# Kernel optimization log

Hardware: AMD Instinct MI355X
Metric: run time of the kernel (lower is better)

## Reference

```python
import jax, jax.numpy as jnp
import numpy as np

ALPHA = 0.2  # LeakyReLU negative slope


def setup_inputs() -> dict:
    key = jax.random.key(0)
    k1, k2, k3, k4 = jax.random.split(key, 4)
    N, Fin, Fout = 8192, 256, 64
    inputs = {
        "input": jax.random.normal(k1, (N, Fin), dtype=jnp.float32),
        "adj": jax.random.randint(k2, (N, N), 0, 2, dtype=jnp.int32),
        "W": jax.random.normal(k3, (Fin, Fout), dtype=jnp.float32) * (1.414 * np.sqrt(2.0 / (Fin + Fout))),
        "a": jax.random.normal(k4, (2 * Fout, 1), dtype=jnp.float32) * (1.414 * np.sqrt(2.0 / (2 * Fout + 1))),
    }
    return inputs


def reference(input, adj, W, a):
    # h: [N, Fout]
    h = input @ W
    Fout = h.shape[1]
    # Decompose pairwise score: e[i,j] = leakyrelu(h[i]@a1 + h[j]@a2)
    # (mathematically identical to the original concat+matmul construction,
    #  but avoids the O(N^2 * 2F) intermediate)
    a1, a2 = a[:Fout, 0], a[Fout:, 0]
    s1 = h @ a1  # [N]
    s2 = h @ a2  # [N]
    e = jax.nn.leaky_relu(s1[:, None] + s2[None, :], negative_slope=ALPHA)  # [N, N]
    # Mask non-edges with -10 (as in the original), row softmax
    masked = jnp.where(adj > 0, e, jnp.float32(-10.0))
    attention = jax.nn.softmax(masked, axis=1)
    # dropout p=0.0 (eval/reference mode): identity
    h_prime = attention @ h  # [N, Fout]
    return jax.nn.elu(h_prime)  # concat=True path
```

## Files before the change

kernel.cpp:

```cpp
#include <hip/hip_runtime.h>
#include <hip/hip_bf16.h>
#include <cstdint>
#include <cstddef>

#define NN 8192
#define FIN 256
#define FOUT 64
#define ALPHA_SLOPE 0.2f
#define EXP_M10 4.5399929762484854e-05f

#define JSPLIT 2
#define JT 1024
#define NTILE ((NN / JSPLIT) / JT)
#define CP 68

typedef short s16x8 __attribute__((ext_vector_type(8)));
typedef float f32x4 __attribute__((ext_vector_type(4)));
typedef int   i32x4 __attribute__((ext_vector_type(4)));

__device__ __forceinline__ unsigned short f2bf(float x) {
    union { float f; uint32_t u; } v; v.f = x;
    uint32_t u = v.u;
    return (unsigned short)((u + 0x7FFFu + ((u >> 16) & 1u)) >> 16);
}

__device__ __forceinline__ int wt_off(int row, int chunk) {
    return row * JT + (((chunk) ^ (row & 7)) << 3);
}

__global__ __launch_bounds__(256) void k_h(
    const float* __restrict__ input, const float* __restrict__ W,
    const float* __restrict__ a,
    unsigned short* __restrict__ htg, float* __restrict__ s1, float* __restrict__ s2)
{
    __shared__ __align__(16) unsigned short tile[64][28];
    const int wid  = threadIdx.x >> 6;
    const int lane = threadIdx.x & 63;
    const int i0   = blockIdx.x * 16;
    const int r0   = wid * 4;
    const float* inb = input + (size_t)(i0 + r0) * FIN;

    float acc0 = 0.f, acc1 = 0.f, acc2 = 0.f, acc3 = 0.f;
    #pragma unroll 4
    for (int c = 0; c < FIN; c += 4) {
        float w0 = W[(c + 0) * FOUT + lane];
        float w1 = W[(c + 1) * FOUT + lane];
        float w2 = W[(c + 2) * FOUT + lane];
        float w3 = W[(c + 3) * FOUT + lane];
        float4 x0 = *(const float4*)(inb + 0 * FIN + c);
        float4 x1 = *(const float4*)(inb + 1 * FIN + c);
        float4 x2 = *(const float4*)(inb + 2 * FIN + c);
        float4 x3 = *(const float4*)(inb + 3 * FIN + c);
        acc0 = fmaf(x0.x, w0, fmaf(x0.y, w1, fmaf(x0.z, w2, fmaf(x0.w, w3, acc0))));
        acc1 = fmaf(x1.x, w0, fmaf(x1.y, w1, fmaf(x1.z, w2, fmaf(x1.w, w3, acc1))));
        acc2 = fmaf(x2.x, w0, fmaf(x2.y, w1, fmaf(x2.z, w2, fmaf(x2.w, w3, acc2))));
        acc3 = fmaf(x3.x, w0, fmaf(x3.y, w1, fmaf(x3.z, w2, fmaf(x3.w, w3, acc3))));
    }

    const float a1v = a[lane], a2v = a[FOUT + lane];
    float accs[4] = {acc0, acc1, acc2, acc3};
    #pragma unroll
    for (int r = 0; r < 4; ++r) {
        float v1 = accs[r] * a1v;
        float v2 = accs[r] * a2v;
        #pragma unroll
        for (int off = 32; off; off >>= 1) {
            v1 += __shfl_xor(v1, off);
            v2 += __shfl_xor(v2, off);
        }
        if (lane == 0) { s1[i0 + r0 + r] = v1; s2[i0 + r0 + r] = v2; }
        tile[lane][r0 + r] = f2bf(accs[r]);
    }
    __syncthreads();

    const int feat = threadIdx.x >> 2;
    const int cg   = (threadIdx.x & 3) * 4;
    uint2 q = *(const uint2*)&tile[feat][cg];
    *(uint2*)(htg + (size_t)feat * NN + i0 + cg) = q;
}

__global__ __launch_bounds__(256, 4) void k_attn(
    const int* __restrict__ adj,
    const unsigned short* __restrict__ htg,
    const float* __restrict__ s1g, const float* __restrict__ s2g,
    float* __restrict__ slabs)
{
    __shared__ __align__(16) unsigned short Wt[16 * JT];

    const int t    = threadIdx.x;
    const int wid  = t >> 6;
    const int lane = t & 63;
    const int bi   = blockIdx.x >> 1;
    const int js   = blockIdx.x & 1;
    const int i0   = bi * 16;
    const int jbase = js * (NN / JSPLIT);
    const int m    = lane & 15;
    const int quad = lane >> 4;

    const int srow = wid * 4;
    float s1r[4];
    #pragma unroll
    for (int r = 0; r < 4; ++r) s1r[r] = s1g[i0 + srow + r];

    const int kq = wid * (JT / 4);

    const short bd = (m == 0) ? (short)0x3F80 : (short)0;
    const s16x8 bden = {bd, bd, bd, bd, bd, bd, bd, bd};

    f32x4 acc0 = {0,0,0,0}, acc1 = {0,0,0,0}, acc2 = {0,0,0,0},
          acc3 = {0,0,0,0}, acc4 = {0,0,0,0};

    for (int tile = 0; tile < NTILE; ++tile) {
        const int j0 = jbase + tile * JT;
        __syncthreads();

        #pragma unroll
        for (int rr = 0; rr < 4; ++rr) {
            const int row = srow + rr;
            const int* ap = adj + (size_t)(i0 + row) * NN + j0;
            const float s1v = s1r[rr];
            #pragma unroll
            for (int c = 0; c < 4; ++c) {
                const int cc = c * 256 + lane * 4;
                i32x4  av = *(const i32x4*)(ap + cc);
                float4 sv = *(const float4*)(s2g + j0 + cc);
                float x0 = s1v + sv.x, x1 = s1v + sv.y;
                float x2 = s1v + sv.z, x3 = s1v + sv.w;
                float w0 = (av.x > 0) ? __expf(fmaxf(x0, ALPHA_SLOPE * x0)) : EXP_M10;
                float w1 = (av.y > 0) ? __expf(fmaxf(x1, ALPHA_SLOPE * x1)) : EXP_M10;
                float w2 = (av.z > 0) ? __expf(fmaxf(x2, ALPHA_SLOPE * x2)) : EXP_M10;
                float w3 = (av.w > 0) ? __expf(fmaxf(x3, ALPHA_SLOPE * x3)) : EXP_M10;
                uint2 pk;
                pk.x = (unsigned int)f2bf(w0) | ((unsigned int)f2bf(w1) << 16);
                pk.y = (unsigned int)f2bf(w2) | ((unsigned int)f2bf(w3) << 16);
                const int chunk = c * 32 + (lane >> 1);
                *(uint2*)&Wt[wt_off(row, chunk) + (lane & 1) * 4] = pk;
            }
        }
        __syncthreads();

        #pragma unroll
        for (int ks = 0; ks < 8; ++ks) {
            const int kc = kq + ks * 32;
            s16x8 af = *(const s16x8*)&Wt[wt_off(m, (kc >> 3) + quad)];
            const unsigned short* hp = htg + (size_t)m * NN + j0 + kc + quad * 8;
            s16x8 b0 = *(const s16x8*)(hp);
            s16x8 b1 = *(const s16x8*)(hp + (size_t)16 * NN);
            s16x8 b2 = *(const s16x8*)(hp + (size_t)32 * NN);
            s16x8 b3 = *(const s16x8*)(hp + (size_t)48 * NN);
            acc0 = __builtin_amdgcn_mfma_f32_16x16x32_bf16(af, b0,   acc0, 0, 0, 0);
            acc1 = __builtin_amdgcn_mfma_f32_16x16x32_bf16(af, b1,   acc1, 0, 0, 0);
            acc2 = __builtin_amdgcn_mfma_f32_16x16x32_bf16(af, b2,   acc2, 0, 0, 0);
            acc3 = __builtin_amdgcn_mfma_f32_16x16x32_bf16(af, b3,   acc3, 0, 0, 0);
            acc4 = __builtin_amdgcn_mfma_f32_16x16x32_bf16(af, bden, acc4, 0, 0, 0);
        }
    }

    __syncthreads();
    float* red = (float*)Wt;
    float* myred = red + wid * 16 * CP;
    #pragma unroll
    for (int reg = 0; reg < 4; ++reg) {
        const int r = quad * 4 + reg;
        myred[r * CP +  0 + m] = acc0[reg];
        myred[r * CP + 16 + m] = acc1[reg];
        myred[r * CP + 32 + m] = acc2[reg];
        myred[r * CP + 48 + m] = acc3[reg];
        if (m == 0) myred[r * CP + 64] = acc4[reg];
    }
    __syncthreads();

    float* slab = slabs + (size_t)js * ((size_t)NN * CP);
    for (int idx = t; idx < 16 * 65; idx += 256) {
        const int r = idx / 65, c = idx % 65;
        float s = red[0 * 16 * CP + r * CP + c] + red[1 * 16 * CP + r * CP + c]
                + red[2 * 16 * CP + r * CP + c] + red[3 * 16 * CP + r * CP + c];
        slab[(size_t)(i0 + r) * CP + c] = s;
    }
}

__global__ __launch_bounds__(256) void k_norm(
    const float* __restrict__ slabs, float* __restrict__ out)
{
    int gid = blockIdx.x * 256 + threadIdx.x;
    int i = gid >> 6, k = gid & 63;
    float num = 0.f, den = 0.f;
    #pragma unroll
    for (int js = 0; js < JSPLIT; ++js) {
        const float* row = slabs + (size_t)js * ((size_t)NN * CP) + (size_t)i * CP;
        num += row[k];
        den += row[64];
    }
    float v = num / den;
    out[gid] = (v > 0.f) ? v : (__expf(v) - 1.f);
}

extern "C" void kernel_launch(void* const* d_in, const int* in_sizes, int n_in,
                              void* d_out, int out_size, void* d_ws, size_t ws_size,
                              hipStream_t stream) {
    const float* input = (const float*)d_in[0];
    const int*   adj   = (const int*)d_in[1];
    const float* W     = (const float*)d_in[2];
    const float* a     = (const float*)d_in[3];
    float* out = (float*)d_out;

    char* ws = (char*)d_ws;
    float* slabs = (float*)ws;
    size_t off = (size_t)JSPLIT * NN * CP * sizeof(float);
    unsigned short* htg = (unsigned short*)(ws + off);
    off += (size_t)FOUT * NN * sizeof(unsigned short);
    float* s1 = (float*)(ws + off); off += NN * sizeof(float);
    float* s2 = (float*)(ws + off);

    k_h   <<<NN / 16, 256, 0, stream>>>(input, W, a, htg, s1, s2);
    k_attn<<<(NN / 16) * JSPLIT, 256, 0, stream>>>(adj, htg, s1, s2, slabs);
    k_norm<<<NN * FOUT / 256, 256, 0, stream>>>(slabs, out);
}
```

Baseline: 443.6 us.

## Split attention into separate score materialization and PV matmul kernels

Moves computation of the masked exp scores out of the attention matmul kernel into a standalone elementwise kernel. That kernel writes a full N×N bf16 weight matrix to workspace in a swizzled layout. The PV kernel then only streams the precomputed weights into LDS and runs the MFMA accumulation. The aim is to decouple the exp/adj-bound stage from the matmul stage for better parallelism and occupancy, at the cost of an extra 128 MB write and read through global memory.

```diff
diff --git a/kernel.cpp b/kernel.cpp
--- a/kernel.cpp
+++ b/kernel.cpp
@@ -10,8 +10,6 @@
 #define EXP_M10 4.5399929762484854e-05f
 
 #define JSPLIT 2
-#define JT 1024
-#define NTILE ((NN / JSPLIT) / JT)
 #define CP 68
 
 typedef short s16x8 __attribute__((ext_vector_type(8)));
@@ -22,10 +20,6 @@
     union { float f; uint32_t u; } v; v.f = x;
     uint32_t u = v.u;
     return (unsigned short)((u + 0x7FFFu + ((u >> 16) & 1u)) >> 16);
-}
-
-__device__ __forceinline__ int wt_off(int row, int chunk) {
-    return row * JT + (((chunk) ^ (row & 7)) << 3);
 }
 
 __global__ __launch_bounds__(256) void k_h(
@@ -79,13 +73,72 @@
     *(uint2*)(htg + (size_t)feat * NN + i0 + cg) = q;
 }
 
-__global__ __launch_bounds__(256, 4) void k_attn(
+__global__ __launch_bounds__(256) void k_score(
     const int* __restrict__ adj,
+    const float* __restrict__ s1g, const float* __restrict__ s2g,
+    unsigned short* __restrict__ wg)
+{
+    const int tid = blockIdx.x * 256 + threadIdx.x;
+    #pragma unroll 2
+    for (int s = 0; s < 8; ++s) {
+        const size_t base = ((size_t)s * 524288 + tid) * 16;
+        const int i = (int)(base >> 13);
+        const int j = (int)(base & 8191);
+        const float s1v = s1g[i];
+        const int*   ap  = adj + base;
+        const float* s2p = s2g + j;
+
+        i32x4 a0 = *(const i32x4*)(ap + 0);
+        i32x4 a1 = *(const i32x4*)(ap + 4);
+        i32x4 a2 = *(const i32x4*)(ap + 8);
+        i32x4 a3 = *(const i32x4*)(ap + 12);
+        float4 v0 = *(const float4*)(s2p + 0);
+        float4 v1 = *(const float4*)(s2p + 4);
+        float4 v2 = *(const float4*)(s2p + 8);
+        float4 v3 = *(const float4*)(s2p + 12);
+
+        float w[16];
+        {
+            float xs[16] = {
+                s1v+v0.x, s1v+v0.y, s1v+v0.z, s1v+v0.w,
+                s1v+v1.x, s1v+v1.y, s1v+v1.z, s1v+v1.w,
+                s1v+v2.x, s1v+v2.y, s1v+v2.z, s1v+v2.w,
+                s1v+v3.x, s1v+v3.y, s1v+v3.z, s1v+v3.w };
+            int ad[16] = {
+                a0.x,a0.y,a0.z,a0.w, a1.x,a1.y,a1.z,a1.w,
+                a2.x,a2.y,a2.z,a2.w, a3.x,a3.y,a3.z,a3.w };
+            #pragma unroll
+            for (int e = 0; e < 16; ++e) {
+                float x = xs[e];
+                w[e] = (ad[e] > 0) ? __expf(fmaxf(x, ALPHA_SLOPE * x)) : EXP_M10;
+            }
+        }
+
+        uint4 pk0, pk1;
+        pk0.x = (unsigned)f2bf(w[0])  | ((unsigned)f2bf(w[1])  << 16);
+        pk0.y = (unsigned)f2bf(w[2])  | ((unsigned)f2bf(w[3])  << 16);
+        pk0.z = (unsigned)f2bf(w[4])  | ((unsigned)f2bf(w[5])  << 16);
+        pk0.w = (unsigned)f2bf(w[6])  | ((unsigned)f2bf(w[7])  << 16);
+        pk1.x = (unsigned)f2bf(w[8])  | ((unsigned)f2bf(w[9])  << 16);
+        pk1.y = (unsigned)f2bf(w[10]) | ((unsigned)f2bf(w[11]) << 16);
+        pk1.z = (unsigned)f2bf(w[12]) | ((unsigned)f2bf(w[13]) << 16);
+        pk1.w = (unsigned)f2bf(w[14]) | ((unsigned)f2bf(w[15]) << 16);
+
+        const int x7 = i & 7;
+        const int c0 = j >> 3;
+        unsigned short* rowp = wg + (size_t)i * NN;
+        *(uint4*)(rowp + (size_t)(c0       ^ x7) * 8) = pk0;
+        *(uint4*)(rowp + (size_t)((c0 + 1) ^ x7) * 8) = pk1;
+    }
+}
+
+__global__ __launch_bounds__(256) void k_pv(
+    const unsigned short* __restrict__ wg,
     const unsigned short* __restrict__ htg,
-    const float* __restrict__ s1g, const float* __restrict__ s2g,
     float* __restrict__ slabs)
 {
-    __shared__ __align__(16) unsigned short Wt[16 * JT];
+    __shared__ __align__(16) unsigned char smem[18432];
+    unsigned short* Wt = (unsigned short*)smem;
 
     const int t    = threadIdx.x;
     const int wid  = t >> 6;
@@ -97,53 +150,31 @@
     const int m    = lane & 15;
     const int quad = lane >> 4;
 
-    const int srow = wid * 4;
-    float s1r[4];
-    #pragma unroll
-    for (int r = 0; r < 4; ++r) s1r[r] = s1g[i0 + srow + r];
-
-    const int kq = wid * (JT / 4);
-
     const short bd = (m == 0) ? (short)0x3F80 : (short)0;
     const s16x8 bden = {bd, bd, bd, bd, bd, bd, bd, bd};
 
     f32x4 acc0 = {0,0,0,0}, acc1 = {0,0,0,0}, acc2 = {0,0,0,0},
           acc3 = {0,0,0,0}, acc4 = {0,0,0,0};
 
-    for (int tile = 0; tile < NTILE; ++tile) {
-        const int j0 = jbase + tile * JT;
+    for (int tile = 0; tile < 8; ++tile) {
+        const int j0 = jbase + tile * 512;
         __syncthreads();
 
         #pragma unroll
         for (int rr = 0; rr < 4; ++rr) {
-            const int row = srow + rr;
-            const int* ap = adj + (size_t)(i0 + row) * NN + j0;
-            const float s1v = s1r[rr];
-            #pragma unroll
-            for (int c = 0; c < 4; ++c) {
-                const int cc = c * 256 + lane * 4;
-                i32x4  av = *(const i32x4*)(ap + cc);
-                float4 sv = *(const float4*)(s2g + j0 + cc);
-                float x0 = s1v + sv.x, x1 = s1v + sv.y;
-                float x2 = s1v + sv.z, x3 = s1v + sv.w;
-                float w0 = (av.x > 0) ? __expf(fmaxf(x0, ALPHA_SLOPE * x0)) : EXP_M10;
-                float w1 = (av.y > 0) ? __expf(fmaxf(x1, ALPHA_SLOPE * x1)) : EXP_M10;
-                float w2 = (av.z > 0) ? __expf(fmaxf(x2, ALPHA_SLOPE * x2)) : EXP_M10;
-                float w3 = (av.w > 0) ? __expf(fmaxf(x3, ALPHA_SLOPE * x3)) : EXP_M10;
-                uint2 pk;
-                pk.x = (unsigned int)f2bf(w0) | ((unsigned int)f2bf(w1) << 16);
-                pk.y = (unsigned int)f2bf(w2) | ((unsigned int)f2bf(w3) << 16);
-                const int chunk = c * 32 + (lane >> 1);
-                *(uint2*)&Wt[wt_off(row, chunk) + (lane & 1) * 4] = pk;
-            }
+            const int row = wid * 4 + rr;
+            const unsigned short* src = wg + (size_t)(i0 + row) * NN + j0 + lane * 8;
+            s16x8 val = *(const s16x8*)src;
+            *(s16x8*)&Wt[(row * 64 + lane) * 8] = val;
         }
         __syncthreads();
 
         #pragma unroll
-        for (int ks = 0; ks < 8; ++ks) {
-            const int kc = kq + ks * 32;
-            s16x8 af = *(const s16x8*)&Wt[wt_off(m, (kc >> 3) + quad)];
-            const unsigned short* hp = htg + (size_t)m * NN + j0 + kc + quad * 8;
+        for (int kq = 0; kq < 4; ++kq) {
+            const int kk = wid * 4 + kq;
+            const int pos = (kk * 4 + quad) ^ (m & 7);
+            s16x8 af = *(const s16x8*)&Wt[(m * 64 + pos) * 8];
+            const unsigned short* hp = htg + (size_t)m * NN + j0 + kk * 32 + quad * 8;
             s16x8 b0 = *(const s16x8*)(hp);
             s16x8 b1 = *(const s16x8*)(hp + (size_t)16 * NN);
             s16x8 b2 = *(const s16x8*)(hp + (size_t)32 * NN);
@@ -157,7 +188,7 @@
     }
 
     __syncthreads();
-    float* red = (float*)Wt;
+    float* red = (float*)smem;
     float* myred = red + wid * 16 * CP;
     #pragma unroll
     for (int reg = 0; reg < 4; ++reg) {
@@ -205,14 +236,17 @@
     float* out = (float*)d_out;
 
     char* ws = (char*)d_ws;
-    float* slabs = (float*)ws;
-    size_t off = (size_t)JSPLIT * NN * CP * sizeof(float);
+    unsigned short* wg = (unsigned short*)ws;
+    size_t off = (size_t)NN * NN * sizeof(unsigned short);
+    float* slabs = (float*)(ws + off);
+    off += (size_t)JSPLIT * NN * CP * sizeof(float);
     unsigned short* htg = (unsigned short*)(ws + off);
     off += (size_t)FOUT * NN * sizeof(unsigned short);
     float* s1 = (float*)(ws + off); off += NN * sizeof(float);
     float* s2 = (float*)(ws + off);
 
-    k_h   <<<NN / 16, 256, 0, stream>>>(input, W, a, htg, s1, s2);
-    k_attn<<<(NN / 16) * JSPLIT, 256, 0, stream>>>(adj, htg, s1, s2, slabs);
-    k_norm<<<NN * FOUT / 256, 256, 0, stream>>>(slabs, out);
-}
+    k_h    <<<NN / 16, 256, 0, stream>>>(input, W, a, htg, s1, s2);
+    k_score<<<2048, 256, 0, stream>>>(adj, s1, s2, wg);
+    k_pv   <<<(NN / 16) * JSPLIT, 256, 0, stream>>>(wg, htg, slabs);
+    k_norm <<<NN * FOUT / 256, 256, 0, stream>>>(slabs, out);
+}
```

After: 502.6 us. 1.13x slower.

## Double-buffer adjacency tiles via global_load_lds and fuse normalization into attention kernel

Applied to the files above, without the earlier changes.

Streams adjacency rows into shared memory with direct global-to-LDS loads, double-buffered across 512-column tiles so the next tile's load overlaps the current tile's compute. Attention weights are now computed straight from LDS into MFMA A-fragments in registers instead of being written to and re-read from an LDS weight tile. The j-split and the separate normalization kernel are removed, and the division plus ELU are done in the attention epilogue. This halves the grid to 512 blocks, which may lower occupancy and parallelism, and relies on a full waitcnt per tile.

```diff
diff --git a/kernel.cpp b/kernel.cpp
--- a/kernel.cpp
+++ b/kernel.cpp
@@ -9,9 +9,10 @@
 #define ALPHA_SLOPE 0.2f
 #define EXP_M10 4.5399929762484854e-05f
 
-#define JSPLIT 2
-#define JT 1024
-#define NTILE ((NN / JSPLIT) / JT)
+#define TILE_COLS 512
+#define NTILES (NN / TILE_COLS)
+#define ROW_PITCH 2064
+#define BUF_BYTES (16 * ROW_PITCH)
 #define CP 68
 
 typedef short s16x8 __attribute__((ext_vector_type(8)));
@@ -24,8 +25,11 @@
     return (unsigned short)((u + 0x7FFFu + ((u >> 16) & 1u)) >> 16);
 }
 
-__device__ __forceinline__ int wt_off(int row, int chunk) {
-    return row * JT + (((chunk) ^ (row & 7)) << 3);
+__device__ __forceinline__ void gl_lds16(const int* g, void* l) {
+    __builtin_amdgcn_global_load_lds(
+        (const __attribute__((address_space(1))) unsigned int*)g,
+        (__attribute__((address_space(3))) unsigned int*)l,
+        16, 0, 0);
 }
 
 __global__ __launch_bounds__(256) void k_h(
@@ -79,30 +83,22 @@
     *(uint2*)(htg + (size_t)feat * NN + i0 + cg) = q;
 }
 
-__global__ __launch_bounds__(256, 4) void k_attn(
+__global__ __launch_bounds__(256) void k_attn(
     const int* __restrict__ adj,
     const unsigned short* __restrict__ htg,
     const float* __restrict__ s1g, const float* __restrict__ s2g,
-    float* __restrict__ slabs)
+    float* __restrict__ out)
 {
-    __shared__ __align__(16) unsigned short Wt[16 * JT];
+    __shared__ __align__(16) unsigned char smem[2 * BUF_BYTES];
 
     const int t    = threadIdx.x;
     const int wid  = t >> 6;
     const int lane = t & 63;
-    const int bi   = blockIdx.x >> 1;
-    const int js   = blockIdx.x & 1;
-    const int i0   = bi * 16;
-    const int jbase = js * (NN / JSPLIT);
+    const int i0   = blockIdx.x * 16;
     const int m    = lane & 15;
     const int quad = lane >> 4;
 
-    const int srow = wid * 4;
-    float s1r[4];
-    #pragma unroll
-    for (int r = 0; r < 4; ++r) s1r[r] = s1g[i0 + srow + r];
-
-    const int kq = wid * (JT / 4);
+    const float s1v = s1g[i0 + m];
 
     const short bd = (m == 0) ? (short)0x3F80 : (short)0;
     const s16x8 bden = {bd, bd, bd, bd, bd, bd, bd, bd};
@@ -110,54 +106,81 @@
     f32x4 acc0 = {0,0,0,0}, acc1 = {0,0,0,0}, acc2 = {0,0,0,0},
           acc3 = {0,0,0,0}, acc4 = {0,0,0,0};
 
-    for (int tile = 0; tile < NTILE; ++tile) {
-        const int j0 = jbase + tile * JT;
-        __syncthreads();
-
+    {
         #pragma unroll
         for (int rr = 0; rr < 4; ++rr) {
-            const int row = srow + rr;
-            const int* ap = adj + (size_t)(i0 + row) * NN + j0;
-            const float s1v = s1r[rr];
+            const int r = wid * 4 + rr;
+            const int* g = adj + (size_t)(i0 + r) * NN + lane * 4;
+            unsigned char* l = smem + r * ROW_PITCH;
+            gl_lds16(g, l);
+            gl_lds16(g + 256, l + 1024);
+        }
+    }
+    __builtin_amdgcn_s_waitcnt(0);
+    __syncthreads();
+
+    for (int tl = 0; tl < NTILES; ++tl) {
+        const unsigned char* buf = smem + (tl & 1) * BUF_BYTES;
+        const int j0 = tl * TILE_COLS;
+
+        if (tl < NTILES - 1) {
+            unsigned char* nbuf = smem + ((tl + 1) & 1) * BUF_BYTES;
+            const int nj0 = (tl + 1) * TILE_COLS;
             #pragma unroll
-            for (int c = 0; c < 4; ++c) {
-                const int cc = c * 256 + lane * 4;
-                i32x4  av = *(const i32x4*)(ap + cc);
-                float4 sv = *(const float4*)(s2g + j0 + cc);
-                float x0 = s1v + sv.x, x1 = s1v + sv.y;
-                float x2 = s1v + sv.z, x3 = s1v + sv.w;
-                float w0 = (av.x > 0) ? __expf(fmaxf(x0, ALPHA_SLOPE * x0)) : EXP_M10;
-                float w1 = (av.y > 0) ? __expf(fmaxf(x1, ALPHA_SLOPE * x1)) : EXP_M10;
-                float w2 = (av.z > 0) ? __expf(fmaxf(x2, ALPHA_SLOPE * x2)) : EXP_M10;
-                float w3 = (av.w > 0) ? __expf(fmaxf(x3, ALPHA_SLOPE * x3)) : EXP_M10;
-                uint2 pk;
-                pk.x = (unsigned int)f2bf(w0) | ((unsigned int)f2bf(w1) << 16);
-                pk.y = (unsigned int)f2bf(w2) | ((unsigned int)f2bf(w3) << 16);
-                const int chunk = c * 32 + (lane >> 1);
-                *(uint2*)&Wt[wt_off(row, chunk) + (lane & 1) * 4] = pk;
+            for (int rr = 0; rr < 4; ++rr) {
+                const int r = wid * 4 + rr;
+                const int* g = adj + (size_t)(i0 + r) * NN + nj0 + lane * 4;
+                unsigned char* l = nbuf + r * ROW_PITCH;
+                gl_lds16(g, l);
+                gl_lds16(g + 256, l + 1024);
             }
         }
-        __syncthreads();
 
         #pragma unroll
-        for (int ks = 0; ks < 8; ++ks) {
-            const int kc = kq + ks * 32;
-            s16x8 af = *(const s16x8*)&Wt[wt_off(m, (kc >> 3) + quad)];
-            const unsigned short* hp = htg + (size_t)m * NN + j0 + kc + quad * 8;
+        for (int kq = 0; kq < 4; ++kq) {
+            const int kk = wid * 4 + kq;
+            const unsigned char* ap = buf + m * ROW_PITCH + kk * 128 + quad * 32;
+            i32x4 a0 = *(const i32x4*)(ap);
+            i32x4 a1 = *(const i32x4*)(ap + 16);
+
+            const int j = j0 + kk * 32 + quad * 8;
+            float4 sa = *(const float4*)(s2g + j);
+            float4 sb = *(const float4*)(s2g + j + 4);
+            const unsigned short* hp = htg + (size_t)m * NN + j;
             s16x8 b0 = *(const s16x8*)(hp);
             s16x8 b1 = *(const s16x8*)(hp + (size_t)16 * NN);
             s16x8 b2 = *(const s16x8*)(hp + (size_t)32 * NN);
             s16x8 b3 = *(const s16x8*)(hp + (size_t)48 * NN);
+
+            float x0 = s1v + sa.x, x1 = s1v + sa.y, x2 = s1v + sa.z, x3 = s1v + sa.w;
+            float x4 = s1v + sb.x, x5 = s1v + sb.y, x6 = s1v + sb.z, x7 = s1v + sb.w;
+            float w0 = (a0.x > 0) ? __expf(fmaxf(x0, ALPHA_SLOPE * x0)) : EXP_M10;
+            float w1 = (a0.y > 0) ? __expf(fmaxf(x1, ALPHA_SLOPE * x1)) : EXP_M10;
+            float w2 = (a0.z > 0) ? __expf(fmaxf(x2, ALPHA_SLOPE * x2)) : EXP_M10;
+            float w3 = (a0.w > 0) ? __expf(fmaxf(x3, ALPHA_SLOPE * x3)) : EXP_M10;
+            float w4 = (a1.x > 0) ? __expf(fmaxf(x4, ALPHA_SLOPE * x4)) : EXP_M10;
+            float w5 = (a1.y > 0) ? __expf(fmaxf(x5, ALPHA_SLOPE * x5)) : EXP_M10;
+            float w6 = (a1.z > 0) ? __expf(fmaxf(x6, ALPHA_SLOPE * x6)) : EXP_M10;
+            float w7 = (a1.w > 0) ? __expf(fmaxf(x7, ALPHA_SLOPE * x7)) : EXP_M10;
+
+            s16x8 af;
+            af[0] = (short)f2bf(w0); af[1] = (short)f2bf(w1);
+            af[2] = (short)f2bf(w2); af[3] = (short)f2bf(w3);
+            af[4] = (short)f2bf(w4); af[5] = (short)f2bf(w5);
+            af[6] = (short)f2bf(w6); af[7] = (short)f2bf(w7);
+
             acc0 = __builtin_amdgcn_mfma_f32_16x16x32_bf16(af, b0,   acc0, 0, 0, 0);
             acc1 = __builtin_amdgcn_mfma_f32_16x16x32_bf16(af, b1,   acc1, 0, 0, 0);
             acc2 = __builtin_amdgcn_mfma_f32_16x16x32_bf16(af, b2,   acc2, 0, 0, 0);
             acc3 = __builtin_amdgcn_mfma_f32_16x16x32_bf16(af, b3,   acc3, 0, 0, 0);
             acc4 = __builtin_amdgcn_mfma_f32_16x16x32_bf16(af, bden, acc4, 0, 0, 0);
         }
-    }
-
-    __syncthreads();
-    float* red = (float*)Wt;
+
+        __builtin_amdgcn_s_waitcnt(0);
+        __syncthreads();
+    }
+
+    float* red = (float*)smem;
     float* myred = red + wid * 16 * CP;
     #pragma unroll
     for (int reg = 0; reg < 4; ++reg) {
@@ -170,29 +193,16 @@
     }
     __syncthreads();
 
-    float* slab = slabs + (size_t)js * ((size_t)NN * CP);
-    for (int idx = t; idx < 16 * 65; idx += 256) {
-        const int r = idx / 65, c = idx % 65;
-        float s = red[0 * 16 * CP + r * CP + c] + red[1 * 16 * CP + r * CP + c]
-                + red[2 * 16 * CP + r * CP + c] + red[3 * 16 * CP + r * CP + c];
-        slab[(size_t)(i0 + r) * CP + c] = s;
-    }
-}
-
-__global__ __launch_bounds__(256) void k_norm(
-    const float* __restrict__ slabs, float* __restrict__ out)
-{
-    int gid = blockIdx.x * 256 + threadIdx.x;
-    int i = gid >> 6, k = gid & 63;
-    float num = 0.f, den = 0.f;
     #pragma unroll
-    for (int js = 0; js < JSPLIT; ++js) {
-        const float* row = slabs + (size_t)js * ((size_t)NN * CP) + (size_t)i * CP;
-        num += row[k];
-        den += row[64];
-    }
-    float v = num / den;
-    out[gid] = (v > 0.f) ? v : (__expf(v) - 1.f);
+    for (int idx = t; idx < 16 * 64; idx += 256) {
+        const int r = idx >> 6, c = idx & 63;
+        float num = red[0 * 16 * CP + r * CP + c] + red[1 * 16 * CP + r * CP + c]
+                  + red[2 * 16 * CP + r * CP + c] + red[3 * 16 * CP + r * CP + c];
+        float den = red[0 * 16 * CP + r * CP + 64] + red[1 * 16 * CP + r * CP + 64]
+                  + red[2 * 16 * CP + r * CP + 64] + red[3 * 16 * CP + r * CP + 64];
+        float v = num / den;
+        out[(size_t)(i0 + r) * FOUT + c] = (v > 0.f) ? v : (__expf(v) - 1.f);
+    }
 }
 
 extern "C" void kernel_launch(void* const* d_in, const int* in_sizes, int n_in,
@@ -205,14 +215,11 @@
     float* out = (float*)d_out;
 
     char* ws = (char*)d_ws;
-    float* slabs = (float*)ws;
-    size_t off = (size_t)JSPLIT * NN * CP * sizeof(float);
-    unsigned short* htg = (unsigned short*)(ws + off);
-    off += (size_t)FOUT * NN * sizeof(unsigned short);
+    unsigned short* htg = (unsigned short*)ws;
+    size_t off = (size_t)FOUT * NN * sizeof(unsigned short);
     float* s1 = (float*)(ws + off); off += NN * sizeof(float);
     float* s2 = (float*)(ws + off);
 
     k_h   <<<NN / 16, 256, 0, stream>>>(input, W, a, htg, s1, s2);
-    k_attn<<<(NN / 16) * JSPLIT, 256, 0, stream>>>(adj, htg, s1, s2, slabs);
-    k_norm<<<NN * FOUT / 256, 256, 0, stream>>>(slabs, out);
-}
+    k_attn<<<NN / 16, 256, 0, stream>>>(adj, htg, s1, s2, out);
+}
```

New measurement: 419.2 us. -5.5%, faster.

## Double-buffer attention strips in LDS and stage h tiles with 512-thread blocks

Applied to the files above, without the earlier changes.

The attention kernel now processes 128-column strips with double-buffered LDS for both the bf16 attention weights and a staged copy of h. The next strip's adj, s2 and h loads are issued before the current strip's MFMAs, so global latency can overlap with compute. Blocks grow to 32 rows and 512 threads, with waves split by row group, K half and feature half. h now comes from LDS instead of being read directly from global per wave, which cuts redundant h traffic but adds a barrier per strip and more register pressure.

```diff
diff --git a/kernel.cpp b/kernel.cpp
--- a/kernel.cpp
+++ b/kernel.cpp
@@ -10,8 +10,10 @@
 #define EXP_M10 4.5399929762484854e-05f
 
 #define JSPLIT 2
-#define JT 1024
-#define NTILE ((NN / JSPLIT) / JT)
+#define STRIP 128
+#define NSTRIP ((NN / JSPLIT) / STRIP)
+#define WPITCH 272
+#define HPITCH 272
 #define CP 68
 
 typedef short s16x8 __attribute__((ext_vector_type(8)));
@@ -24,8 +26,8 @@
     return (unsigned short)((u + 0x7FFFu + ((u >> 16) & 1u)) >> 16);
 }
 
-__device__ __forceinline__ int wt_off(int row, int chunk) {
-    return row * JT + (((chunk) ^ (row & 7)) << 3);
+__device__ __forceinline__ unsigned int pk2(float lo, float hi) {
+    return (unsigned int)f2bf(lo) | ((unsigned int)f2bf(hi) << 16);
 }
 
 __global__ __launch_bounds__(256) void k_h(
@@ -79,103 +81,146 @@
     *(uint2*)(htg + (size_t)feat * NN + i0 + cg) = q;
 }
 
-__global__ __launch_bounds__(256, 4) void k_attn(
+__global__ __launch_bounds__(512, 4) void k_attn(
     const int* __restrict__ adj,
     const unsigned short* __restrict__ htg,
     const float* __restrict__ s1g, const float* __restrict__ s2g,
     float* __restrict__ slabs)
 {
-    __shared__ __align__(16) unsigned short Wt[16 * JT];
+    __shared__ __align__(16) unsigned char wbuf[2][32 * WPITCH];
+    __shared__ __align__(16) unsigned char hbuf[2][64 * HPITCH];
 
     const int t    = threadIdx.x;
     const int wid  = t >> 6;
     const int lane = t & 63;
     const int bi   = blockIdx.x >> 1;
     const int js   = blockIdx.x & 1;
-    const int i0   = bi * 16;
+    const int i0   = bi * 32;
     const int jbase = js * (NN / JSPLIT);
     const int m    = lane & 15;
     const int quad = lane >> 4;
-
-    const int srow = wid * 4;
-    float s1r[4];
-    #pragma unroll
-    for (int r = 0; r < 4; ++r) s1r[r] = s1g[i0 + srow + r];
-
-    const int kq = wid * (JT / 4);
+    const int rg   = wid >> 2;
+    const int kp   = (wid >> 1) & 1;
+    const int fg   = wid & 1;
+
+    const int srow  = t >> 4;
+    const int scol  = (t & 15) * 8;
+    const int sfeat = t >> 3;
+    const int scol2 = (t & 7) * 16;
+    const float s1v = s1g[i0 + srow];
 
     const short bd = (m == 0) ? (short)0x3F80 : (short)0;
     const s16x8 bden = {bd, bd, bd, bd, bd, bd, bd, bd};
 
-    f32x4 acc0 = {0,0,0,0}, acc1 = {0,0,0,0}, acc2 = {0,0,0,0},
-          acc3 = {0,0,0,0}, acc4 = {0,0,0,0};
-
-    for (int tile = 0; tile < NTILE; ++tile) {
-        const int j0 = jbase + tile * JT;
+    f32x4 accA = {0,0,0,0}, accB = {0,0,0,0}, accD = {0,0,0,0};
+
+    const int* adjrow = adj + (size_t)(i0 + srow) * NN + jbase;
+    const unsigned short* hrow = htg + (size_t)sfeat * NN + jbase;
+
+    {
+        i32x4  a0 = *(const i32x4*)(adjrow + scol);
+        i32x4  a1 = *(const i32x4*)(adjrow + scol + 4);
+        float4 v0 = *(const float4*)(s2g + jbase + scol);
+        float4 v1 = *(const float4*)(s2g + jbase + scol + 4);
+        s16x8  h0 = *(const s16x8*)(hrow + scol2);
+        s16x8  h1 = *(const s16x8*)(hrow + scol2 + 8);
+
+        float x0=s1v+v0.x, x1=s1v+v0.y, x2=s1v+v0.z, x3=s1v+v0.w;
+        float x4=s1v+v1.x, x5=s1v+v1.y, x6=s1v+v1.z, x7=s1v+v1.w;
+        float w0=(a0.x>0)?__expf(fmaxf(x0,ALPHA_SLOPE*x0)):EXP_M10;
+        float w1=(a0.y>0)?__expf(fmaxf(x1,ALPHA_SLOPE*x1)):EXP_M10;
+        float w2=(a0.z>0)?__expf(fmaxf(x2,ALPHA_SLOPE*x2)):EXP_M10;
+        float w3=(a0.w>0)?__expf(fmaxf(x3,ALPHA_SLOPE*x3)):EXP_M10;
+        float w4=(a1.x>0)?__expf(fmaxf(x4,ALPHA_SLOPE*x4)):EXP_M10;
+        float w5=(a1.y>0)?__expf(fmaxf(x5,ALPHA_SLOPE*x5)):EXP_M10;
+        float w6=(a1.z>0)?__expf(fmaxf(x6,ALPHA_SLOPE*x6)):EXP_M10;
+        float w7=(a1.w>0)?__expf(fmaxf(x7,ALPHA_SLOPE*x7)):EXP_M10;
+        uint4 pk = { pk2(w0,w1), pk2(w2,w3), pk2(w4,w5), pk2(w6,w7) };
+        *(uint4*)&wbuf[0][srow * WPITCH + scol * 2] = pk;
+        *(s16x8*)&hbuf[0][sfeat * HPITCH + scol2 * 2] = h0;
+        *(s16x8*)&hbuf[0][sfeat * HPITCH + scol2 * 2 + 16] = h1;
+    }
+    __syncthreads();
+
+    for (int s = 0; s < NSTRIP; ++s) {
+        const int cur = s & 1, nxt = cur ^ 1;
+        const bool more = (s + 1 < NSTRIP);
+
+        i32x4 a0, a1; float4 v0, v1; s16x8 h0, h1;
+        if (more) {
+            const int j0n = (s + 1) * STRIP;
+            a0 = *(const i32x4*)(adjrow + j0n + scol);
+            a1 = *(const i32x4*)(adjrow + j0n + scol + 4);
+            v0 = *(const float4*)(s2g + jbase + j0n + scol);
+            v1 = *(const float4*)(s2g + jbase + j0n + scol + 4);
+            h0 = *(const s16x8*)(hrow + j0n + scol2);
+            h1 = *(const s16x8*)(hrow + j0n + scol2 + 8);
+        }
+
+        #pragma unroll
+        for (int kq = 0; kq < 2; ++kq) {
+            const int kk = kp * 2 + kq;
+            const int cb = (kk * 32 + quad * 8) * 2;
+            s16x8 af = *(const s16x8*)&wbuf[cur][(rg * 16 + m) * WPITCH + cb];
+            const unsigned char* hb = &hbuf[cur][cb];
+            if (fg == 0) {
+                s16x8 b0 = *(const s16x8*)(hb + (m +  0) * HPITCH);
+                s16x8 b1 = *(const s16x8*)(hb + (m + 16) * HPITCH);
+                accA = __builtin_amdgcn_mfma_f32_16x16x32_bf16(af, b0, accA, 0, 0, 0);
+                accB = __builtin_amdgcn_mfma_f32_16x16x32_bf16(af, b1, accB, 0, 0, 0);
+            } else {
+                s16x8 b2 = *(const s16x8*)(hb + (m + 32) * HPITCH);
+                s16x8 b3 = *(const s16x8*)(hb + (m + 48) * HPITCH);
+                accA = __builtin_amdgcn_mfma_f32_16x16x32_bf16(af, b2,   accA, 0, 0, 0);
+                accB = __builtin_amdgcn_mfma_f32_16x16x32_bf16(af, b3,   accB, 0, 0, 0);
+                accD = __builtin_amdgcn_mfma_f32_16x16x32_bf16(af, bden, accD, 0, 0, 0);
+            }
+        }
+
+        if (more) {
+            float x0=s1v+v0.x, x1=s1v+v0.y, x2=s1v+v0.z, x3=s1v+v0.w;
+            float x4=s1v+v1.x, x5=s1v+v1.y, x6=s1v+v1.z, x7=s1v+v1.w;
+            float w0=(a0.x>0)?__expf(fmaxf(x0,ALPHA_SLOPE*x0)):EXP_M10;
+            float w1=(a0.y>0)?__expf(fmaxf(x1,ALPHA_SLOPE*x1)):EXP_M10;
+            float w2=(a0.z>0)?__expf(fmaxf(x2,ALPHA_SLOPE*x2)):EXP_M10;
+            float w3=(a0.w>0)?__expf(fmaxf(x3,ALPHA_SLOPE*x3)):EXP_M10;
+            float w4=(a1.x>0)?__expf(fmaxf(x4,ALPHA_SLOPE*x4)):EXP_M10;
+            float w5=(a1.y>0)?__expf(fmaxf(x5,ALPHA_SLOPE*x5)):EXP_M10;
+            float w6=(a1.z>0)?__expf(fmaxf(x6,ALPHA_SLOPE*x6)):EXP_M10;
+            float w7=(a1.w>0)?__expf(fmaxf(x7,ALPHA_SLOPE*x7)):EXP_M10;
+            uint4 pk = { pk2(w0,w1), pk2(w2,w3), pk2(w4,w5), pk2(w6,w7) };
+            *(uint4*)&wbuf[nxt][srow * WPITCH + scol * 2] = pk;
+            *(s16x8*)&hbuf[nxt][sfeat * HPITCH + scol2 * 2] = h0;
+            *(s16x8*)&hbuf[nxt][sfeat * HPITCH + scol2 * 2 + 16] = h1;
+        }
         __syncthreads();
-
-        #pragma unroll
-        for (int rr = 0; rr < 4; ++rr) {
-            const int row = srow + rr;
-            const int* ap = adj + (size_t)(i0 + row) * NN + j0;
-            const float s1v = s1r[rr];
-            #pragma unroll
-            for (int c = 0; c < 4; ++c) {
-                const int cc = c * 256 + lane * 4;
-                i32x4  av = *(const i32x4*)(ap + cc);
-                float4 sv = *(const float4*)(s2g + j0 + cc);
-                float x0 = s1v + sv.x, x1 = s1v + sv.y;
-                float x2 = s1v + sv.z, x3 = s1v + sv.w;
-                float w0 = (av.x > 0) ? __expf(fmaxf(x0, ALPHA_SLOPE * x0)) : EXP_M10;
-                float w1 = (av.y > 0) ? __expf(fmaxf(x1, ALPHA_SLOPE * x1)) : EXP_M10;
-                float w2 = (av.z > 0) ? __expf(fmaxf(x2, ALPHA_SLOPE * x2)) : EXP_M10;
-                float w3 = (av.w > 0) ? __expf(fmaxf(x3, ALPHA_SLOPE * x3)) : EXP_M10;
-                uint2 pk;
-                pk.x = (unsigned int)f2bf(w0) | ((unsigned int)f2bf(w1) << 16);
-                pk.y = (unsigned int)f2bf(w2) | ((unsigned int)f2bf(w3) << 16);
-                const int chunk = c * 32 + (lane >> 1);
-                *(uint2*)&Wt[wt_off(row, chunk) + (lane & 1) * 4] = pk;
-            }
-        }
-        __syncthreads();
-
-        #pragma unroll
-        for (int ks = 0; ks < 8; ++ks) {
-            const int kc = kq + ks * 32;
-            s16x8 af = *(const s16x8*)&Wt[wt_off(m, (kc >> 3) + quad)];
-            const unsigned short* hp = htg + (size_t)m * NN + j0 + kc + quad * 8;
-            s16x8 b0 = *(const s16x8*)(hp);
-            s16x8 b1 = *(const s16x8*)(hp + (size_t)16 * NN);
-            s16x8 b2 = *(const s16x8*)(hp + (size_t)32 * NN);
-            s16x8 b3 = *(const s16x8*)(hp + (size_t)48 * NN);
-            acc0 = __builtin_amdgcn_mfma_f32_16x16x32_bf16(af, b0,   acc0, 0, 0, 0);
-            acc1 = __builtin_amdgcn_mfma_f32_16x16x32_bf16(af, b1,   acc1, 0, 0, 0);
-            acc2 = __builtin_amdgcn_mfma_f32_16x16x32_bf16(af, b2,   acc2, 0, 0, 0);
-            acc3 = __builtin_amdgcn_mfma_f32_16x16x32_bf16(af, b3,   acc3, 0, 0, 0);
-            acc4 = __builtin_amdgcn_mfma_f32_16x16x32_bf16(af, bden, acc4, 0, 0, 0);
-        }
-    }
-
-    __syncthreads();
-    float* red = (float*)Wt;
-    float* myred = red + wid * 16 * CP;
+    }
+
+    float* red = (float*)hbuf;
+    float* myr = red + wid * (16 * 34);
     #pragma unroll
     for (int reg = 0; reg < 4; ++reg) {
         const int r = quad * 4 + reg;
-        myred[r * CP +  0 + m] = acc0[reg];
-        myred[r * CP + 16 + m] = acc1[reg];
-        myred[r * CP + 32 + m] = acc2[reg];
-        myred[r * CP + 48 + m] = acc3[reg];
-        if (m == 0) myred[r * CP + 64] = acc4[reg];
+        myr[r * 34 + m]      = accA[reg];
+        myr[r * 34 + 16 + m] = accB[reg];
+        if (fg == 1 && m == 0) myr[r * 34 + 32] = accD[reg];
     }
     __syncthreads();
 
     float* slab = slabs + (size_t)js * ((size_t)NN * CP);
-    for (int idx = t; idx < 16 * 65; idx += 256) {
-        const int r = idx / 65, c = idx % 65;
-        float s = red[0 * 16 * CP + r * CP + c] + red[1 * 16 * CP + r * CP + c]
-                + red[2 * 16 * CP + r * CP + c] + red[3 * 16 * CP + r * CP + c];
-        slab[(size_t)(i0 + r) * CP + c] = s;
+    #pragma unroll
+    for (int idx = t; idx < 32 * 64; idx += 512) {
+        const int r = idx >> 6, c = idx & 63;
+        const int rg2 = r >> 4, rr = r & 15;
+        const int fg2 = c >> 5, lc = c & 31;
+        float num = red[(rg2 * 4 + 0 + fg2) * 544 + rr * 34 + lc]
+                  + red[(rg2 * 4 + 2 + fg2) * 544 + rr * 34 + lc];
+        slab[(size_t)(i0 + r) * CP + c] = num;
+        if (c == 0) {
+            float den = red[(rg2 * 4 + 1) * 544 + rr * 34 + 32]
+                      + red[(rg2 * 4 + 3) * 544 + rr * 34 + 32];
+            slab[(size_t)(i0 + r) * CP + 64] = den;
+        }
     }
 }
 
@@ -213,6 +258,6 @@
     float* s2 = (float*)(ws + off);
 
     k_h   <<<NN / 16, 256, 0, stream>>>(input, W, a, htg, s1, s2);
-    k_attn<<<(NN / 16) * JSPLIT, 256, 0, stream>>>(adj, htg, s1, s2, slabs);
+    k_attn<<<(NN / 32) * JSPLIT, 512, 0, stream>>>(adj, htg, s1, s2, slabs);
     k_norm<<<NN * FOUT / 256, 256, 0, stream>>>(slabs, out);
 }
```

Result: faster. 391.3 us (-11.8%).
